# Optimization experiments

Hardware: AMD Instinct MI355X
Metric: run time of the kernel (lower is better)

The kernel has to match this reference:

```python
import jax, jax.numpy as jnp
import numpy as np

N, E, H, IN = 4096, 65536, 256, 16
N_BLOCKS, N_SUB = 3, 2
IE = 2 * H + 2  # edge-mlp input: h[row] ++ h[col] ++ edge_attr(2)
NORM_FACTOR = 100.0


def setup_inputs() -> dict:
    key = jax.random.key(0)
    ks = jax.random.split(key, 24)
    G = N_BLOCKS * N_SUB  # 6 GCLs total

    def p(k, shape, fan_in, gain=1.0):
        return gain * jax.random.normal(k, shape, jnp.float32) / np.sqrt(fan_in)

    return {
        "h": jax.random.normal(ks[0], (N, IN), jnp.float32),
        "x": jax.random.normal(ks[1], (N, 3), jnp.float32),
        "edge_index": jax.random.randint(ks[2], (2, E), 0, N),
        # embedding in/out
        "emb_w": p(ks[3], (IN, H), IN), "emb_b": jnp.zeros((H,), jnp.float32),
        "out_w": p(ks[4], (H, IN), H), "out_b": jnp.zeros((IN,), jnp.float32),
        # GCL edge MLP (stacked over the 6 GCLs)
        "edge_w1": p(ks[5], (G, IE, H), IE), "edge_b1": jnp.zeros((G, H), jnp.float32),
        "edge_w2": p(ks[6], (G, H, H), H), "edge_b2": jnp.zeros((G, H), jnp.float32),
        # GCL node MLP
        "node_w1": p(ks[7], (G, 2 * H, H), 2 * H), "node_b1": jnp.zeros((G, H), jnp.float32),
        "node_w2": p(ks[8], (G, H, H), H), "node_b2": jnp.zeros((G, H), jnp.float32),
        # EquivariantUpdate coord MLP (stacked over 3 blocks); last layer xavier gain=0.001, no bias
        "coord_w1": p(ks[9], (N_BLOCKS, IE, H), IE), "coord_b1": jnp.zeros((N_BLOCKS, H), jnp.float32),
        "coord_w2": p(ks[10], (N_BLOCKS, H, H), H), "coord_b2": jnp.zeros((N_BLOCKS, H), jnp.float32),
        "coord_w3": p(ks[11], (N_BLOCKS, H, 1), H, gain=0.001),
    }


def reference(h, x, edge_index, emb_w, emb_b, out_w, out_b,
              edge_w1, edge_b1, edge_w2, edge_b2,
              node_w1, node_b1, node_w2, node_b2,
              coord_w1, coord_b1, coord_w2, coord_b2, coord_w3):
    row, col = edge_index[0], edge_index[1]
    n_nodes = h.shape[0]

    def seg_sum(data):  # unsorted_segment_sum with 'sum' aggregation / normalization_factor
        return jax.ops.segment_sum(data, row, num_segments=n_nodes) / NORM_FACTOR

    def coord2diff(xc):  # norm_constant = 1
        d = xc[row] - xc[col]                      # [E,3]
        radial = jnp.sum(d * d, axis=1, keepdims=True)  # [E,1]
        cd = d / (jnp.sqrt(radial + 1e-8) + 1.0)
        return radial, cd

    dist0, _ = coord2diff(x)          # EGNN-level distances (from initial coords)
    h = h @ emb_w + emb_b             # node embedding

    gi = 0
    for b in range(N_BLOCKS):
        radial, coord_diff = coord2diff(x)
        ea = jnp.concatenate([radial, dist0], axis=1)   # [E,2] edge_attr
        for _ in range(N_SUB):  # GCL sublayers
            m = jnp.concatenate([h[row], h[col], ea], axis=1)           # [E, 2H+2]
            m = jax.nn.silu(m @ edge_w1[gi] + edge_b1[gi])
            m = jax.nn.silu(m @ edge_w2[gi] + edge_b2[gi])              # [E, H]
            agg = seg_sum(m)                                            # [N, H]
            u = jnp.concatenate([h, agg], axis=1)                       # [N, 2H]
            u = jax.nn.silu(u @ node_w1[gi] + node_b1[gi])
            h = h + u @ node_w2[gi] + node_b2[gi]                       # residual node update
            gi += 1
        # EquivariantUpdate (tanh=False)
        t = jnp.concatenate([h[row], h[col], ea], axis=1)
        t = jax.nn.silu(t @ coord_w1[b] + coord_b1[b])
        t = jax.nn.silu(t @ coord_w2[b] + coord_b2[b])
        trans = coord_diff * (t @ coord_w3[b])                          # [E,3]
        x = x + seg_sum(trans)

    h = h @ out_w + out_b
    return h, x
```

## Files before the change

### kernel.cpp

```cpp
#include <hip/hip_runtime.h>
#include <hip/hip_bf16.h>
#include <cstdint>
#include <cstddef>

#define NN 4096
#define NE 65536
#define HD 256

typedef __attribute__((ext_vector_type(4))) float f32x4;
typedef __attribute__((ext_vector_type(8))) __bf16 bf16x8;

static __device__ __forceinline__ float silu_f(float v) {
  float e = __builtin_amdgcn_exp2f(v * -1.442695040888963f);
  return v * __builtin_amdgcn_rcpf(1.f + e);
}

struct TJob { const float* src; __bf16* dst; int K; int N; };
struct TJobs { TJob j[39]; };

__global__ __launch_bounds__(256) void k_transpose(TJobs jobs) {
  TJob jb = jobs.j[blockIdx.z];
  int k0 = blockIdx.x << 5, n0 = blockIdx.y << 5;
  if (k0 >= jb.K || n0 >= jb.N) return;
  __shared__ float t[32][33];
  int tx = threadIdx.x & 31, ty = threadIdx.x >> 5;
#pragma unroll
  for (int r = ty; r < 32; r += 8)
    t[r][tx] = jb.src[(size_t)(k0 + r) * jb.N + n0 + tx];
  __syncthreads();
#pragma unroll
  for (int r = ty; r < 32; r += 8)
    jb.dst[(size_t)(n0 + r) * jb.K + k0 + tx] = (__bf16)t[tx][r];
}

__global__ __launch_bounds__(256) void k_hist(const int* __restrict__ ei, int* __restrict__ cnt) {
  int e = blockIdx.x * 256 + threadIdx.x;
  atomicAdd(&cnt[ei[e]], 1);
}

__global__ __launch_bounds__(1024) void k_scan(const int* __restrict__ cnt, int* __restrict__ offs,
                                               int* __restrict__ cursor) {
  __shared__ int tmp[1024];
  int tid = threadIdx.x;
  int v[4]; int s = 0;
#pragma unroll
  for (int i = 0; i < 4; i++) { v[i] = cnt[tid * 4 + i]; s += v[i]; }
  tmp[tid] = s;
  __syncthreads();
  for (int o = 1; o < 1024; o <<= 1) {
    int t = (tid >= o) ? tmp[tid - o] : 0;
    __syncthreads();
    tmp[tid] += t;
    __syncthreads();
  }
  int base = (tid > 0) ? tmp[tid - 1] : 0;
#pragma unroll
  for (int i = 0; i < 4; i++) {
    offs[tid * 4 + i] = base; cursor[tid * 4 + i] = base; base += v[i];
  }
  if (tid == 1023) offs[4096] = base;
}

__global__ __launch_bounds__(256) void k_scatter(const int* __restrict__ ei, int* __restrict__ cursor,
                                                 int* __restrict__ elist) {
  int e = blockIdx.x * 256 + threadIdx.x;
  int pos = atomicAdd(&cursor[ei[e]], 1);
  elist[pos] = e;
}

__global__ __launch_bounds__(256) void k_csrinit(const int* __restrict__ elist, const int* __restrict__ ei,
                                                 const float* __restrict__ x, int* __restrict__ rowp,
                                                 int* __restrict__ colp, float* __restrict__ d0p,
                                                 float* __restrict__ xc) {
  int i = blockIdx.x * 256 + threadIdx.x;
  if (i < NN * 3) xc[i] = x[i];
  int e = elist[i];
  int r = ei[e], c = ei[NE + e];
  rowp[i] = r; colp[i] = c;
  float dx = x[r * 3 + 0] - x[c * 3 + 0];
  float dy = x[r * 3 + 1] - x[c * 3 + 1];
  float dz = x[r * 3 + 2] - x[c * 3 + 2];
  d0p[i] = dx * dx + dy * dy + dz * dz;
}

__global__ __launch_bounds__(256) void k_geo(const int* __restrict__ rowp, const int* __restrict__ colp,
                                             const float* __restrict__ x, float* __restrict__ radp,
                                             float* __restrict__ cdp) {
  int i = blockIdx.x * 256 + threadIdx.x;
  int r = rowp[i], c = colp[i];
  float dx = x[r * 3 + 0] - x[c * 3 + 0];
  float dy = x[r * 3 + 1] - x[c * 3 + 1];
  float dz = x[r * 3 + 2] - x[c * 3 + 2];
  float rad = dx * dx + dy * dy + dz * dz;
  radp[i] = rad;
  float inv = 1.f / (sqrtf(rad + 1e-8f) + 1.f);
  cdp[i * 3 + 0] = dx * inv; cdp[i * 3 + 1] = dy * inv; cdp[i * 3 + 2] = dz * inv;
}

__global__ __launch_bounds__(256) void k_embed(const float* __restrict__ h0, const float* __restrict__ W,
                                               const float* __restrict__ b, float* __restrict__ hf,
                                               __bf16* __restrict__ h16) {
  int n = blockIdx.x, c = threadIdx.x;
  float s = b[c];
#pragma unroll
  for (int i = 0; i < 16; i++) s += h0[n * 16 + i] * W[i * 256 + c];
  hf[(size_t)n * HD + c] = s;
  h16[(size_t)n * HD + c] = (__bf16)s;
}

__global__ __launch_bounds__(256) void k_mkbias(const float* __restrict__ eb1, const float* __restrict__ cb1,
                                                float* __restrict__ bias512) {
  int i = blockIdx.x * 256 + threadIdx.x;
  int g = i >> 9, r = i & 511;
  float v = 0.f;
  if (r < 256) v = (g < 6) ? eb1[g * 256 + r] : cb1[(g - 6) * 256 + r];
  bias512[i] = v;
}

__global__ __launch_bounds__(256) void k_segsum(const __bf16* __restrict__ m2p, const int* __restrict__ offs,
                                                __bf16* __restrict__ agg16) {
  __shared__ float sd[8][256];
  int n = blockIdx.x, t = threadIdx.x;
  int g = t >> 5, l = t & 31;
  int c0 = l << 3;
  float a[8] = {};
  int ib = offs[n], ie = offs[n + 1];
  for (int i = ib + g; i < ie; i += 8) {
    bf16x8 v = *(const bf16x8*)(m2p + (size_t)i * 256 + c0);
#pragma unroll
    for (int j = 0; j < 8; j++) a[j] += (float)v[j];
  }
#pragma unroll
  for (int j = 0; j < 8; j++) sd[g][c0 + j] = a[j];
  __syncthreads();
  float s = 0.f;
#pragma unroll
  for (int j = 0; j < 8; j++) s += sd[j][t];
  agg16[(size_t)n * 256 + t] = (__bf16)(s * 0.01f);
}

__global__ __launch_bounds__(256) void k_xupd(const float* __restrict__ transp, const int* __restrict__ offs,
                                              float* __restrict__ xc) {
  int n = blockIdx.x * 256 + threadIdx.x;
  if (n >= NN) return;
  float a0 = 0.f, a1 = 0.f, a2 = 0.f;
  int i1 = offs[n + 1];
  for (int i = offs[n]; i < i1; i++) {
    a0 += transp[i * 3 + 0]; a1 += transp[i * 3 + 1]; a2 += transp[i * 3 + 2];
  }
  xc[n * 3 + 0] += a0 * 0.01f;
  xc[n * 3 + 1] += a1 * 0.01f;
  xc[n * 3 + 2] += a2 * 0.01f;
}

__global__ __launch_bounds__(256) void k_out(const float* __restrict__ hf, const float* __restrict__ W,
                                             const float* __restrict__ b, const float* __restrict__ xc,
                                             float* __restrict__ out) {
  int t = blockIdx.x * 256 + threadIdx.x;
  if (blockIdx.x < 256) {
    int n = t >> 4, j = t & 15;
    float s = b[j];
    for (int c = 0; c < 256; c++) s += hf[(size_t)n * HD + c] * W[c * 16 + j];
    out[n * 16 + j] = s;
  } else {
    int i = t - NN * 16;
    if (i < NN * 3) out[NN * 16 + i] = xc[i];
  }
}

template <int EPI>
__global__ __launch_bounds__(256, 4) void k_edgeblk(
    const __bf16* __restrict__ PQ, const int* __restrict__ rowp, const int* __restrict__ colp,
    const float* __restrict__ radp, const float* __restrict__ d0p,
    const float* __restrict__ w1r, const float* __restrict__ w1d,
    const __bf16* __restrict__ Bt, const float* __restrict__ b2,
    __bf16* __restrict__ m2p,
    const float* __restrict__ w3, const float* __restrict__ cdp, float* __restrict__ transp) {
  __shared__ alignas(16) char smem[36864];
  float*  wgt = (float*)smem;
  __bf16* Bs0 = (__bf16*)(smem + 4096);
  __bf16* Bs1 = (__bf16*)(smem + 4096 + 16384);
  float*  reds = (float*)(smem + 4096);

  const int tid = threadIdx.x;
  const int lane = tid & 63;
  const int w = tid >> 6;
  const int l15 = lane & 15;
  const int kg = lane >> 4;
  const int R0 = blockIdx.x * 64;
  const int rowg = R0 + w * 16 + l15;

  const __bf16* pBase = PQ + (size_t)rowp[rowg] * 512;
  const __bf16* qBase = PQ + (size_t)colp[rowg] * 512 + 256;
  const float rad = radp[rowg], dd0 = d0p[rowg];

  wgt[tid]       = w1r[tid];
  wgt[256 + tid] = w1d[tid];
  wgt[512 + tid] = b2[tid];
  if (EPI == 1) wgt[768 + tid] = w3[tid];

  int srcOff[4], ldsOff[4];
#pragma unroll
  for (int q = 0; q < 4; q++) {
    int s = q * 256 + tid;
    int n = s >> 2, g = s & 3;
    srcOff[q] = n * 256 + ((g ^ ((n >> 1) & 3)) << 3);
    ldsOff[q] = s * 8;
  }

  uint4 rb[4];
#pragma unroll
  for (int q = 0; q < 4; q++) rb[q] = *(const uint4*)(Bt + srcOff[q]);
  bf16x8 pvc = *(const bf16x8*)(pBase + kg * 8);
  bf16x8 qvc = *(const bf16x8*)(qBase + kg * 8);
#pragma unroll
  for (int q = 0; q < 4; q++) *(uint4*)&Bs0[ldsOff[q]] = rb[q];
  __syncthreads();

  f32x4 acc[16] = {};

#pragma unroll
  for (int t = 0; t < 8; t++) {
    const __bf16* Bcur = (t & 1) ? Bs1 : Bs0;
    __bf16*       Bnxt = (t & 1) ? Bs0 : Bs1;
    bf16x8 pvn, qvn;
    if (t < 7) {
      int kt = (t + 1) * 32;
#pragma unroll
      for (int q = 0; q < 4; q++) rb[q] = *(const uint4*)(Bt + kt + srcOff[q]);
      pvn = *(const bf16x8*)(pBase + kt + kg * 8);
      qvn = *(const bf16x8*)(qBase + kt + kg * 8);
    }
    const int k0 = t * 32 + kg * 8;
    f32x4 wr0 = *(const f32x4*)&wgt[k0],       wr1 = *(const f32x4*)&wgt[k0 + 4];
    f32x4 wd0 = *(const f32x4*)&wgt[256 + k0], wd1 = *(const f32x4*)&wgt[256 + k0 + 4];
    bf16x8 af;
#pragma unroll
    for (int j = 0; j < 4; j++)
      af[j] = (__bf16)silu_f((float)pvc[j] + (float)qvc[j] + rad * wr0[j] + dd0 * wd0[j]);
#pragma unroll
    for (int j = 0; j < 4; j++)
      af[4 + j] = (__bf16)silu_f((float)pvc[4 + j] + (float)qvc[4 + j] + rad * wr1[j] + dd0 * wd1[j]);
#pragma unroll
    for (int fn = 0; fn < 16; fn++) {
      int n = fn * 16 + l15;
      bf16x8 bf = *(const bf16x8*)&Bcur[n * 32 + ((kg ^ ((n >> 1) & 3)) << 3)];
      acc[fn] = __builtin_amdgcn_mfma_f32_16x16x32_bf16(af, bf, acc[fn], 0, 0, 0);
    }
    if (t < 7) {
#pragma unroll
      for (int q = 0; q < 4; q++) *(uint4*)&Bnxt[ldsOff[q]] = rb[q];
      pvc = pvn; qvc = qvn;
    }
    __syncthreads();
  }

  if (EPI == 0) {
    __bf16* ep = (__bf16*)(smem + 4096 + w * 4224);
#pragma unroll
    for (int p = 0; p < 2; p++) {
      if ((kg >> 1) == p) {
        int rl = (kg & 1) * 4;
#pragma unroll
        for (int fn = 0; fn < 16; fn++) {
          int col = fn * 16 + l15;
          float bv = wgt[512 + col];
#pragma unroll
          for (int j = 0; j < 4; j++)
            ep[(rl + j) * 264 + col] = (__bf16)silu_f(acc[fn][j] + bv);
        }
      }
      __syncthreads();
#pragma unroll
      for (int i = 0; i < 4; i++) {
        int r = i * 2 + (lane >> 5);
        int g = lane & 31;
        uint4 v = *(const uint4*)&ep[r * 264 + g * 8];
        *(uint4*)(m2p + ((size_t)(R0 + w * 16 + p * 8 + r)) * 256 + g * 8) = v;
      }
      __syncthreads();
    }
  } else {
    float s[4] = {0.f, 0.f, 0.f, 0.f};
#pragma unroll
    for (int fn = 0; fn < 16; fn++) {
      int col = fn * 16 + l15;
      float bv = wgt[512 + col], wv = wgt[768 + col];
#pragma unroll
      for (int j = 0; j < 4; j++)
        s[j] += silu_f(acc[fn][j] + bv) * wv;
    }
#pragma unroll
    for (int off = 1; off < 16; off <<= 1)
#pragma unroll
      for (int j = 0; j < 4; j++)
        s[j] += __shfl_xor(s[j], off, 64);
    __syncthreads();
    if (l15 == 0) {
#pragma unroll
      for (int j = 0; j < 4; j++)
        reds[w * 16 + kg * 4 + j] = s[j];
    }
    __syncthreads();
    if (tid < 64) {
      float sv = reds[tid];
      size_t i = (size_t)R0 + tid;
      transp[i * 3 + 0] = cdp[i * 3 + 0] * sv;
      transp[i * 3 + 1] = cdp[i * 3 + 1] * sv;
      transp[i * 3 + 2] = cdp[i * 3 + 2] * sv;
    }
  }
}

template <int EPI, int SPLIT>
__global__ __launch_bounds__(256) void k_gemm64(const __bf16* __restrict__ A, const __bf16* __restrict__ A2,
                                                const __bf16* __restrict__ Bt,
                                                const float* __restrict__ bias, __bf16* __restrict__ outb,
                                                float* __restrict__ outf, int M, int N, int K) {
  constexpr int BM = 64, BN = 64, BK = 64;
  __shared__ __bf16 As[2][BM * BK];
  __shared__ __bf16 Bs[2][BN * BK];
  const int tid = threadIdx.x;
  const int lane = tid & 63;
  const int wave = tid >> 6;
  const int wm = wave >> 1, wn = wave & 1;
  const size_t m0 = (size_t)blockIdx.x * BM;
  const size_t n0 = (size_t)blockIdx.y * BN;
  const int r0 = tid >> 3, g0 = tid & 7;
  const int gs0 = (g0 ^ (r0 & 7)) << 3;
  const int Astride = SPLIT ? 256 : K;

  f32x4 acc[2][2] = {};
  const int NT = K >> 6;

  {
    uint4 a0 = *(const uint4*)(A + (m0 + r0) * Astride + g0 * 8);
    uint4 a1 = *(const uint4*)(A + (m0 + r0 + 32) * Astride + g0 * 8);
    uint4 b0 = *(const uint4*)(Bt + (n0 + r0) * K + g0 * 8);
    uint4 b1 = *(const uint4*)(Bt + (n0 + r0 + 32) * K + g0 * 8);
    *(uint4*)&As[0][r0 * BK + gs0] = a0;
    *(uint4*)&As[0][(r0 + 32) * BK + gs0] = a1;
    *(uint4*)&Bs[0][r0 * BK + gs0] = b0;
    *(uint4*)&Bs[0][(r0 + 32) * BK + gs0] = b1;
  }
  __syncthreads();

  int buf = 0;
  for (int t = 0; t < NT; ++t) {
    const bool has = (t + 1 < NT);
    uint4 a0, a1, b0, b1;
    if (has) {
      int kt = (t + 1) << 6;
      const __bf16* Ab;
      int ko;
      if (SPLIT) { Ab = (kt < 256) ? A : A2; ko = kt & 255; }
      else       { Ab = A; ko = kt; }
      a0 = *(const uint4*)(Ab + (m0 + r0) * Astride + ko + g0 * 8);
      a1 = *(const uint4*)(Ab + (m0 + r0 + 32) * Astride + ko + g0 * 8);
      b0 = *(const uint4*)(Bt + (n0 + r0) * K + kt + g0 * 8);
      b1 = *(const uint4*)(Bt + (n0 + r0 + 32) * K + kt + g0 * 8);
    }
#pragma unroll
    for (int ks = 0; ks < BK; ks += 32) {
      const int kg = (ks >> 3) + (lane >> 4);
      bf16x8 af[2], bfv[2];
#pragma unroll
      for (int fm = 0; fm < 2; fm++) {
        int r = wm * 32 + fm * 16 + (lane & 15);
        af[fm] = *(const bf16x8*)&As[buf][r * BK + ((kg ^ (r & 7)) << 3)];
      }
#pragma unroll
      for (int fn = 0; fn < 2; fn++) {
        int r = wn * 32 + fn * 16 + (lane & 15);
        bfv[fn] = *(const bf16x8*)&Bs[buf][r * BK + ((kg ^ (r & 7)) << 3)];
      }
#pragma unroll
      for (int fm = 0; fm < 2; fm++)
#pragma unroll
        for (int fn = 0; fn < 2; fn++)
          acc[fm][fn] = __builtin_amdgcn_mfma_f32_16x16x32_bf16(af[fm], bfv[fn], acc[fm][fn], 0, 0, 0);
    }
    if (has) {
      *(uint4*)&As[buf ^ 1][r0 * BK + gs0] = a0;
      *(uint4*)&As[buf ^ 1][(r0 + 32) * BK + gs0] = a1;
      *(uint4*)&Bs[buf ^ 1][r0 * BK + gs0] = b0;
      *(uint4*)&Bs[buf ^ 1][(r0 + 32) * BK + gs0] = b1;
    }
    __syncthreads();
    buf ^= 1;
  }

#pragma unroll
  for (int fm = 0; fm < 2; fm++) {
#pragma unroll
    for (int fn = 0; fn < 2; fn++) {
      const size_t col = n0 + wn * 32 + fn * 16 + (lane & 15);
      float bv = (EPI == 4) ? 0.f : bias[col];
#pragma unroll
      for (int j = 0; j < 4; j++) {
        size_t row = m0 + wm * 32 + fm * 16 + ((lane >> 4) << 2) + j;
        size_t idx = row * (size_t)N + col;
        float v = acc[fm][fn][j] + bv;
        if (EPI == 1) {
          outb[idx] = (__bf16)silu_f(v);
        } else if (EPI == 2) {
          float nh = outf[idx] + v;
          outf[idx] = nh;
          outb[idx] = (__bf16)nh;
        } else {
          outb[idx] = (__bf16)v;
        }
      }
    }
  }
}

extern "C" void kernel_launch(void* const* d_in, const int* in_sizes, int n_in,
                              void* d_out, int out_size, void* d_ws, size_t ws_size,
                              hipStream_t stream) {
  const float* h_in    = (const float*)d_in[0];
  const float* x_in    = (const float*)d_in[1];
  const int*   ei      = (const int*)d_in[2];
  const float* emb_w   = (const float*)d_in[3];
  const float* emb_b   = (const float*)d_in[4];
  const float* out_w   = (const float*)d_in[5];
  const float* out_b   = (const float*)d_in[6];
  const float* edge_w1 = (const float*)d_in[7];
  const float* edge_b1 = (const float*)d_in[8];
  const float* edge_w2 = (const float*)d_in[9];
  const float* edge_b2 = (const float*)d_in[10];
  const float* node_w1 = (const float*)d_in[11];
  const float* node_b1 = (const float*)d_in[12];
  const float* node_w2 = (const float*)d_in[13];
  const float* node_b2 = (const float*)d_in[14];
  const float* coord_w1 = (const float*)d_in[15];
  const float* coord_b1 = (const float*)d_in[16];
  const float* coord_w2 = (const float*)d_in[17];
  const float* coord_b2 = (const float*)d_in[18];
  const float* coord_w3 = (const float*)d_in[19];

  char* p = (char*)d_ws;
  auto alloc = [&](size_t bytes) -> void* {
    void* r = (void*)p;
    p += (bytes + 255) & ~(size_t)255;
    return r;
  };
  __bf16* e1T  = (__bf16*)alloc((size_t)6 * 512 * 256 * 2);
  __bf16* e2T  = (__bf16*)alloc((size_t)6 * 256 * 256 * 2);
  __bf16* n1T  = (__bf16*)alloc((size_t)6 * 256 * 512 * 2);
  __bf16* n2T  = (__bf16*)alloc((size_t)6 * 256 * 256 * 2);
  __bf16* c1T  = (__bf16*)alloc((size_t)3 * 512 * 256 * 2);
  __bf16* c2T  = (__bf16*)alloc((size_t)3 * 256 * 256 * 2);
  __bf16* h16  = (__bf16*)alloc((size_t)NN * HD * 2);
  __bf16* PQ16 = (__bf16*)alloc((size_t)NN * 512 * 2);
  __bf16* m2p  = (__bf16*)alloc((size_t)NE * HD * 2);
  __bf16* agg16 = (__bf16*)alloc((size_t)NN * HD * 2);
  __bf16* u    = (__bf16*)alloc((size_t)NN * HD * 2);
  float* hf    = (float*)alloc((size_t)NN * HD * 4);
  float* xc    = (float*)alloc((size_t)NN * 3 * 4);
  float* d0p   = (float*)alloc((size_t)NE * 4);
  float* radp  = (float*)alloc((size_t)NE * 4);
  float* cdp   = (float*)alloc((size_t)NE * 3 * 4);
  float* transp = (float*)alloc((size_t)NE * 3 * 4);
  float* bias512 = (float*)alloc((size_t)9 * 512 * 4);
  int* cnt     = (int*)alloc((size_t)NN * 4);
  int* offs    = (int*)alloc((size_t)(NN + 1) * 4);
  int* cursor  = (int*)alloc((size_t)NN * 4);
  int* elist   = (int*)alloc((size_t)NE * 4);
  int* rowp    = (int*)alloc((size_t)NE * 4);
  int* colp    = (int*)alloc((size_t)NE * 4);

  TJobs jobs;
  int nj = 0;
  for (int gi = 0; gi < 6; gi++) {
    jobs.j[nj++] = { edge_w1 + (size_t)gi * 514 * 256,             e1T + (size_t)gi * 512 * 256,             256, 256 };
    jobs.j[nj++] = { edge_w1 + (size_t)gi * 514 * 256 + 256 * 256, e1T + (size_t)gi * 512 * 256 + 256 * 256, 256, 256 };
    jobs.j[nj++] = { edge_w2 + (size_t)gi * 256 * 256,             e2T + (size_t)gi * 256 * 256,             256, 256 };
    jobs.j[nj++] = { node_w1 + (size_t)gi * 512 * 256,             n1T + (size_t)gi * 256 * 512,             512, 256 };
    jobs.j[nj++] = { node_w2 + (size_t)gi * 256 * 256,             n2T + (size_t)gi * 256 * 256,             256, 256 };
  }
  for (int b = 0; b < 3; b++) {
    jobs.j[nj++] = { coord_w1 + (size_t)b * 514 * 256,             c1T + (size_t)b * 512 * 256,              256, 256 };
    jobs.j[nj++] = { coord_w1 + (size_t)b * 514 * 256 + 256 * 256, c1T + (size_t)b * 512 * 256 + 256 * 256,  256, 256 };
    jobs.j[nj++] = { coord_w2 + (size_t)b * 256 * 256,             c2T + (size_t)b * 256 * 256,              256, 256 };
  }

  hipMemsetAsync(cnt, 0, (size_t)NN * 4, stream);
  k_transpose<<<dim3(16, 8, 39), 256, 0, stream>>>(jobs);
  k_hist<<<NE / 256, 256, 0, stream>>>(ei, cnt);
  k_scan<<<1, 1024, 0, stream>>>(cnt, offs, cursor);
  k_scatter<<<NE / 256, 256, 0, stream>>>(ei, cursor, elist);
  k_csrinit<<<NE / 256, 256, 0, stream>>>(elist, ei, x_in, rowp, colp, d0p, xc);
  k_mkbias<<<18, 256, 0, stream>>>(edge_b1, coord_b1, bias512);
  k_embed<<<NN, 256, 0, stream>>>(h_in, emb_w, emb_b, hf, h16);

  int gi = 0;
  for (int b = 0; b < 3; b++) {
    k_geo<<<NE / 256, 256, 0, stream>>>(rowp, colp, xc, radp, cdp);
    for (int s = 0; s < 2; s++, gi++) {
      const float* w1 = edge_w1 + (size_t)gi * 514 * 256;
      k_gemm64<5, 0><<<dim3(64, 8), 256, 0, stream>>>(
          h16, nullptr, e1T + (size_t)gi * 512 * 256, bias512 + gi * 512, PQ16, nullptr, NN, 512, 256);
      k_edgeblk<0><<<NE / 64, 256, 0, stream>>>(
          PQ16, rowp, colp, radp, d0p, w1 + 512 * 256, w1 + 513 * 256,
          e2T + (size_t)gi * 256 * 256, edge_b2 + gi * 256, m2p, nullptr, nullptr, nullptr);
      k_segsum<<<NN, 256, 0, stream>>>(m2p, offs, agg16);
      k_gemm64<1, 1><<<dim3(64, 4), 256, 0, stream>>>(
          h16, agg16, n1T + (size_t)gi * 256 * 512, node_b1 + gi * 256, u, nullptr, NN, 256, 512);
      k_gemm64<2, 0><<<dim3(64, 4), 256, 0, stream>>>(
          u, nullptr, n2T + (size_t)gi * 256 * 256, node_b2 + gi * 256, h16, hf, NN, 256, 256);
    }
    const float* w1c = coord_w1 + (size_t)b * 514 * 256;
    k_gemm64<5, 0><<<dim3(64, 8), 256, 0, stream>>>(
        h16, nullptr, c1T + (size_t)b * 512 * 256, bias512 + (6 + b) * 512, PQ16, nullptr, NN, 512, 256);
    k_edgeblk<1><<<NE / 64, 256, 0, stream>>>(
        PQ16, rowp, colp, radp, d0p, w1c + 512 * 256, w1c + 513 * 256,
        c2T + (size_t)b * 256 * 256, coord_b2 + b * 256, nullptr,
        coord_w3 + (size_t)b * 256, cdp, transp);
    k_xupd<<<NN / 256, 256, 0, stream>>>(transp, offs, xc);
  }
  k_out<<<256 + 48, 256, 0, stream>>>(hf, out_w, out_b, xc, (float*)d_out);
}
```

Baseline: 480.7 us.

## Stage edge-MLP weight tiles via direct global-to-LDS loads with 512-thread blocks

The fused edge-MLP kernel now runs 512 threads (8 waves) per block over 128 edges, so each shared weight tile staged in LDS serves twice as many rows. Weight tiles now go straight from global memory to LDS with global_load_lds instead of passing through registers, which removes the register staging and the separate LDS store. The MFMA loop is wrapped in s_setprio to favour the matrix phase. Shared memory grows to fit the epilogue buffers for 8 waves. The 512,4 launch bound may tighten the register budget and lower occupancy.

```diff
diff --git a/kernel.cpp b/kernel.cpp
--- a/kernel.cpp
+++ b/kernel.cpp
@@ -169,14 +169,14 @@
 }
 
 template <int EPI>
-__global__ __launch_bounds__(256, 4) void k_edgeblk(
+__global__ __launch_bounds__(512, 4) void k_edgeblk(
     const __bf16* __restrict__ PQ, const int* __restrict__ rowp, const int* __restrict__ colp,
     const float* __restrict__ radp, const float* __restrict__ d0p,
     const float* __restrict__ w1r, const float* __restrict__ w1d,
     const __bf16* __restrict__ Bt, const float* __restrict__ b2,
     __bf16* __restrict__ m2p,
     const float* __restrict__ w3, const float* __restrict__ cdp, float* __restrict__ transp) {
-  __shared__ alignas(16) char smem[36864];
+  __shared__ alignas(16) char smem[37888];
   float*  wgt = (float*)smem;
   __bf16* Bs0 = (__bf16*)(smem + 4096);
   __bf16* Bs1 = (__bf16*)(smem + 4096 + 16384);
@@ -187,34 +187,38 @@
   const int w = tid >> 6;
   const int l15 = lane & 15;
   const int kg = lane >> 4;
-  const int R0 = blockIdx.x * 64;
+  const int R0 = blockIdx.x * 128;
   const int rowg = R0 + w * 16 + l15;
 
   const __bf16* pBase = PQ + (size_t)rowp[rowg] * 512;
   const __bf16* qBase = PQ + (size_t)colp[rowg] * 512 + 256;
   const float rad = radp[rowg], dd0 = d0p[rowg];
 
-  wgt[tid]       = w1r[tid];
-  wgt[256 + tid] = w1d[tid];
-  wgt[512 + tid] = b2[tid];
-  if (EPI == 1) wgt[768 + tid] = w3[tid];
-
-  int srcOff[4], ldsOff[4];
-#pragma unroll
-  for (int q = 0; q < 4; q++) {
-    int s = q * 256 + tid;
+  if (tid < 256) {
+    wgt[tid]       = w1r[tid];
+    wgt[256 + tid] = w1d[tid];
+  } else {
+    int t2 = tid - 256;
+    wgt[512 + t2] = b2[t2];
+    if (EPI == 1) wgt[768 + t2] = w3[t2];
+  }
+
+  int srcOff[2];
+#pragma unroll
+  for (int q = 0; q < 2; q++) {
+    int s = q * 512 + tid;
     int n = s >> 2, g = s & 3;
     srcOff[q] = n * 256 + ((g ^ ((n >> 1) & 3)) << 3);
-    ldsOff[q] = s * 8;
-  }
-
-  uint4 rb[4];
-#pragma unroll
-  for (int q = 0; q < 4; q++) rb[q] = *(const uint4*)(Bt + srcOff[q]);
+  }
+  const int dstE0 = (0 * 512 + (w << 6)) * 8;
+  const int dstE1 = (1 * 512 + (w << 6)) * 8;
+
+  __builtin_amdgcn_global_load_lds((const unsigned int*)(Bt + srcOff[0]),
+                                   (unsigned int*)(Bs0 + dstE0), 16, 0, 0);
+  __builtin_amdgcn_global_load_lds((const unsigned int*)(Bt + srcOff[1]),
+                                   (unsigned int*)(Bs0 + dstE1), 16, 0, 0);
   bf16x8 pvc = *(const bf16x8*)(pBase + kg * 8);
   bf16x8 qvc = *(const bf16x8*)(qBase + kg * 8);
-#pragma unroll
-  for (int q = 0; q < 4; q++) *(uint4*)&Bs0[ldsOff[q]] = rb[q];
   __syncthreads();
 
   f32x4 acc[16] = {};
@@ -226,8 +230,10 @@
     bf16x8 pvn, qvn;
     if (t < 7) {
       int kt = (t + 1) * 32;
-#pragma unroll
-      for (int q = 0; q < 4; q++) rb[q] = *(const uint4*)(Bt + kt + srcOff[q]);
+      __builtin_amdgcn_global_load_lds((const unsigned int*)(Bt + kt + srcOff[0]),
+                                       (unsigned int*)(Bnxt + dstE0), 16, 0, 0);
+      __builtin_amdgcn_global_load_lds((const unsigned int*)(Bt + kt + srcOff[1]),
+                                       (unsigned int*)(Bnxt + dstE1), 16, 0, 0);
       pvn = *(const bf16x8*)(pBase + kt + kg * 8);
       qvn = *(const bf16x8*)(qBase + kt + kg * 8);
     }
@@ -241,17 +247,15 @@
 #pragma unroll
     for (int j = 0; j < 4; j++)
       af[4 + j] = (__bf16)silu_f((float)pvc[4 + j] + (float)qvc[4 + j] + rad * wr1[j] + dd0 * wd1[j]);
+    __builtin_amdgcn_s_setprio(1);
 #pragma unroll
     for (int fn = 0; fn < 16; fn++) {
       int n = fn * 16 + l15;
       bf16x8 bf = *(const bf16x8*)&Bcur[n * 32 + ((kg ^ ((n >> 1) & 3)) << 3)];
       acc[fn] = __builtin_amdgcn_mfma_f32_16x16x32_bf16(af, bf, acc[fn], 0, 0, 0);
     }
-    if (t < 7) {
-#pragma unroll
-      for (int q = 0; q < 4; q++) *(uint4*)&Bnxt[ldsOff[q]] = rb[q];
-      pvc = pvn; qvc = qvn;
-    }
+    __builtin_amdgcn_s_setprio(0);
+    if (t < 7) { pvc = pvn; qvc = qvn; }
     __syncthreads();
   }
 
@@ -302,7 +306,7 @@
         reds[w * 16 + kg * 4 + j] = s[j];
     }
     __syncthreads();
-    if (tid < 64) {
+    if (tid < 128) {
       float sv = reds[tid];
       size_t i = (size_t)R0 + tid;
       transp[i * 3 + 0] = cdp[i * 3 + 0] * sv;
@@ -501,7 +505,7 @@
       const float* w1 = edge_w1 + (size_t)gi * 514 * 256;
       k_gemm64<5, 0><<<dim3(64, 8), 256, 0, stream>>>(
           h16, nullptr, e1T + (size_t)gi * 512 * 256, bias512 + gi * 512, PQ16, nullptr, NN, 512, 256);
-      k_edgeblk<0><<<NE / 64, 256, 0, stream>>>(
+      k_edgeblk<0><<<NE / 128, 512, 0, stream>>>(
           PQ16, rowp, colp, radp, d0p, w1 + 512 * 256, w1 + 513 * 256,
           e2T + (size_t)gi * 256 * 256, edge_b2 + gi * 256, m2p, nullptr, nullptr, nullptr);
       k_segsum<<<NN, 256, 0, stream>>>(m2p, offs, agg16);
@@ -513,7 +517,7 @@
     const float* w1c = coord_w1 + (size_t)b * 514 * 256;
     k_gemm64<5, 0><<<dim3(64, 8), 256, 0, stream>>>(
         h16, nullptr, c1T + (size_t)b * 512 * 256, bias512 + (6 + b) * 512, PQ16, nullptr, NN, 512, 256);
-    k_edgeblk<1><<<NE / 64, 256, 0, stream>>>(
+    k_edgeblk<1><<<NE / 128, 512, 0, stream>>>(
         PQ16, rowp, colp, radp, d0p, w1c + 512 * 256, w1c + 513 * 256,
         c2T + (size_t)b * 256 * 256, coord_b2 + b * 256, nullptr,
         coord_w3 + (size_t)b * 256, cdp, transp);
```

After: 460.0 us. -4.3%, faster.
